# Kernel optimization log

Hardware: AMD Instinct MI355X
Metric: run time of the kernel (lower is better)

The kernel has to match this reference:

```python
import jax, jax.numpy as jnp
import numpy as np

C = 128; L = 2; LMAX = 3; NB = 8
R_MAX = 5.0; P_CUT = 5.0; AVG_NEI = 16.0
DELTA_K = 0.2; K_CUT = 0.6; NKRBF = 128; DP = 8
B_GRAPHS = 8; N_ATOMS = 3200; N_EDGES = 51200; NEL = 10
SKIP = (2.0 + 1.0) ** -0.5  # skip_connection_factor with use_ewald=True
_LOFLM_NP = np.repeat(np.arange(4), [1, 3, 5, 7])  # l index of each of 16 lm slots
LOFLM = jnp.asarray(_LOFLM_NP)
LM1H = jnp.asarray(np.eye(4, dtype=np.float32)[_LOFLM_NP])  # [16,4] one-hot lm->l


def _k_grid_np():
    r = np.arange(-3, 4)
    g = np.stack(np.meshgrid(r, r, r, indexing='ij'), -1).reshape(-1, 3).astype(np.float32) * DELTA_K
    return g[np.linalg.norm(g, axis=1) <= K_CUT + 1e-6]  # [K,3], K=123


def _k_rbf_np(kg):
    d = np.linalg.norm(kg, axis=1)
    c = np.linspace(0.0, K_CUT, NKRBF).astype(np.float32)
    w = c[1] - c[0]
    return np.exp(-0.5 * ((d[:, None] - c[None, :]) / w) ** 2).astype(np.float32)


def _sph_harm(u):
    # real spherical harmonics, e3nn 'component' normalization, l=0..3 -> 16 comps
    x, y, z = u[:, 0], u[:, 1], u[:, 2]
    s3, s5, s15 = 3.0 ** 0.5, 5.0 ** 0.5, 15.0 ** 0.5
    c70, c105, c42, c7 = 70.0 ** 0.5 / 4.0, 105.0 ** 0.5, 42.0 ** 0.5 / 4.0, 7.0 ** 0.5 / 2.0
    comps = [jnp.ones_like(x),
             s3 * x, s3 * y, s3 * z,
             s15 * x * y, s15 * y * z, 0.5 * s5 * (3 * z * z - 1.0), s15 * x * z, 0.5 * s15 * (x * x - y * y),
             c70 * y * (3 * x * x - y * y), c105 * x * y * z, c42 * y * (5 * z * z - 1.0),
             c7 * z * (5 * z * z - 3.0), c42 * x * (5 * z * z - 1.0), 0.5 * c105 * z * (x * x - y * y),
             c70 * x * (x * x - 3 * y * y)]
    return jnp.stack(comps, axis=-1)


def _radial(r):
    # Bessel basis * polynomial cutoff envelope (p=5)
    n = jnp.arange(1, NB + 1, dtype=r.dtype)
    rb = jnp.sqrt(2.0 / R_MAX) * jnp.sin(n * jnp.pi * r[:, None] / R_MAX) / jnp.maximum(r, 1e-9)[:, None]
    uu = jnp.clip(r / R_MAX, 0.0, 1.0)
    p = P_CUT
    env = 1.0 - (p + 1.0) * (p + 2.0) / 2.0 * uu ** 5 + p * (p + 2.0) * uu ** 6 - p * (p + 1.0) / 2.0 * uu ** 7
    env = env * (r < R_MAX)
    return rb * env[:, None]


def _forward(positions, node_attrs, shifts, edge_index, batch, kgrid, krbf, W_embed, atomic_E, rW1, rb1, rW2, rb2, rW3, rb3, rW4, Wup, w2, w3, Wmix, Wr0, Wr1a, Wr1b, Wdown, WupE, Wpre1, bpre1, Wpre2, bpre2, Wm1, bm1, Wm2, bm2):
    silu = jax.nn.silu
    src, dst = edge_index[0], edge_index[1]
    vec = positions[dst] - positions[src] + shifts            # [E,3]
    r = jnp.linalg.norm(vec, axis=1)
    uvec = vec / jnp.maximum(r, 1e-9)[:, None]
    Y = _sph_harm(uvec)                                       # [E,16]
    ef = _radial(r)                                           # [E,8]
    h = node_attrs @ W_embed                                  # [N,C]
    e0 = jax.ops.segment_sum(node_attrs @ atomic_E, batch, num_segments=B_GRAPHS)
    # Ewald precompute (shared across layers, as in the torch code: dot/sinc computed once)
    dot = positions @ kgrid.T                                 # [N,K]
    sd = jnp.prod(jnp.sinc(0.5 * DELTA_K * positions), axis=1, keepdims=True)  # [N,1]
    cosd = sd * jnp.cos(dot)
    sind = sd * jnp.sin(dot)
    kdown = krbf @ Wdown                                      # [K,DP]
    energy = e0
    for i in range(L):
        # ---- Ewald block ----
        hres = h + silu(h @ Wpre1[i] + bpre1[i]) @ Wpre2[i] + bpre2[i]
        kfilter = kdown @ WupE[i]                             # [K,C]
        sfr = jax.ops.segment_sum(hres[:, None, :] * cosd[:, :, None], batch, num_segments=B_GRAPHS)  # [B,K,C]
        sfi = jax.ops.segment_sum(hres[:, None, :] * sind[:, :, None], batch, num_segments=B_GRAPHS)
        he = 0.01 * (jnp.einsum('nk,nkc->nc', cosd, (sfr * kfilter)[batch])
                     + jnp.einsum('nk,nkc->nc', sind, (sfi * kfilter)[batch]))
        he = silu(he @ Wm1[i] + bm1[i])
        he = silu(he @ Wm2[i] + bm2[i])
        # ---- equivariant interaction (channelwise TP with SH, radial-MLP weights) ----
        hu = h @ Wup[i]
        w = silu(ef @ rW1[i] + rb1[i])
        w = silu(w @ rW2[i] + rb2[i])
        w = silu(w @ rW3[i] + rb3[i])
        w = (w @ rW4[i]).reshape(-1, C, LMAX + 1)             # [E,C,4] per-(channel,l) weights
        we = jnp.take(w, LOFLM, axis=2)                       # [E,C,16]
        msg = we * hu[src][:, :, None] * Y[:, None, :]        # [E,C,16]
        A = jax.ops.segment_sum(msg, dst, num_segments=positions.shape[0]) / AVG_NEI  # [N,C,16]
        # ---- product basis (invariant contractions up to correlation 3) + residual sc ----
        scal = A[:, :, 0]
        inv2 = jnp.einsum('ncs,sl->ncl', A * A, LM1H)         # [N,C,4] per-l norms
        feats = scal + jnp.einsum('ncl,lc->nc', inv2, w2[i]) + scal * jnp.einsum('ncl,lc->nc', inv2, w3[i])
        hprod = feats @ Wmix[i] + h
        h = SKIP * (hprod + he)
        # ---- readout ----
        if i < L - 1:
            node_e = (h @ Wr0)[:, 0]
        else:
            node_e = (silu(h @ Wr1a) @ Wr1b)[:, 0]
        energy = energy + jax.ops.segment_sum(node_e, batch, num_segments=B_GRAPHS)
    return energy  # [B]


def setup_inputs() -> dict:
    ks = jax.random.split(jax.random.key(0), 32)
    def rn(i, shape, scale):
        return jax.random.normal(ks[i], shape, jnp.float32) * scale
    d = {}
    d['positions'] = jax.random.normal(ks[0], (N_ATOMS, 3), jnp.float32)
    d['node_attrs'] = jax.random.uniform(ks[1], (N_ATOMS, NEL), dtype=jnp.float32)
    d['shifts'] = jnp.zeros((N_EDGES, 3), jnp.float32)
    d['edge_index'] = jax.random.randint(ks[2], (2, N_EDGES), 0, N_ATOMS)
    d['batch'] = jnp.sort(jax.random.randint(ks[3], (N_ATOMS,), 0, B_GRAPHS))
    kg = _k_grid_np()
    d['kgrid'] = jnp.asarray(kg)
    d['krbf'] = jnp.asarray(_k_rbf_np(kg))
    d['W_embed'] = rn(4, (NEL, C), NEL ** -0.5)
    d['atomic_E'] = rn(5, (NEL,), 1.0)
    d['rW1'] = rn(6, (L, NB, 64), NB ** -0.5)
    d['rb1'] = jnp.zeros((L, 64), jnp.float32)
    d['rW2'] = rn(7, (L, 64, 64), 64 ** -0.5)
    d['rb2'] = jnp.zeros((L, 64), jnp.float32)
    d['rW3'] = rn(8, (L, 64, 64), 64 ** -0.5)
    d['rb3'] = jnp.zeros((L, 64), jnp.float32)
    d['rW4'] = rn(9, (L, 64, C * (LMAX + 1)), 64 ** -0.5)
    d['Wup'] = rn(10, (L, C, C), C ** -0.5)
    d['w2'] = rn(11, (L, LMAX + 1, C), 0.1)
    d['w3'] = rn(12, (L, LMAX + 1, C), 0.1)
    d['Wmix'] = rn(13, (L, C, C), C ** -0.5)
    d['Wr0'] = rn(14, (C, 1), C ** -0.5)
    d['Wr1a'] = rn(15, (C, 16), C ** -0.5)
    d['Wr1b'] = rn(16, (16, 1), 16 ** -0.5)
    d['Wdown'] = rn(17, (NKRBF, DP), NKRBF ** -0.5)
    d['WupE'] = rn(18, (L, DP, C), DP ** -0.5)
    d['Wpre1'] = rn(19, (L, C, C), C ** -0.5)
    d['bpre1'] = jnp.zeros((L, C), jnp.float32)
    d['Wpre2'] = rn(20, (L, C, C), C ** -0.5)
    d['bpre2'] = jnp.zeros((L, C), jnp.float32)
    d['Wm1'] = rn(21, (L, C, C), C ** -0.5)
    d['bm1'] = jnp.zeros((L, C), jnp.float32)
    d['Wm2'] = rn(22, (L, C, C), C ** -0.5)
    d['bm2'] = jnp.zeros((L, C), jnp.float32)
    return d


def reference(positions, node_attrs, shifts, edge_index, batch, kgrid, krbf, W_embed, atomic_E, rW1, rb1, rW2, rb2, rW3, rb3, rW4, Wup, w2, w3, Wmix, Wr0, Wr1a, Wr1b, Wdown, WupE, Wpre1, bpre1, Wpre2, bpre2, Wm1, bm1, Wm2, bm2):
    return _forward(positions, node_attrs, shifts, edge_index, batch, kgrid, krbf, W_embed, atomic_E, rW1, rb1, rW2, rb2, rW3, rb3, rW4, Wup, w2, w3, Wmix, Wr0, Wr1a, Wr1b, Wdown, WupE, Wpre1, bpre1, Wpre2, bpre2, Wm1, bm1, Wm2, bm2)
```

## Files before the change

### kernel.cpp

```cpp
#include <hip/hip_runtime.h>
#include <hip/hip_bf16.h>
#include <math.h>

constexpr int NA  = 3200;
constexpr int NE  = 51200;
constexpr int C   = 128;
constexpr int NK  = 123;
constexpr int NKP = 128;
constexpr int BG  = 8;
constexpr int SFSPLIT = 8;
constexpr float SKIPF = 0.57735026918962576f;
constexpr float AVGN  = 16.0f;
constexpr size_t SFSZ = (size_t)BG * NK * C;

__device__ __forceinline__ float dsilu(float x) { return x / (1.0f + expf(-x)); }

__device__ __forceinline__ unsigned short f2bf(float f) {
    unsigned int u = __float_as_uint(f);
    unsigned int r = (u + 0x7fffu + ((u >> 16) & 1u)) >> 16;
    return (unsigned short)r;
}
__device__ __forceinline__ float bf2f(unsigned short s) {
    return __uint_as_float(((unsigned int)s) << 16);
}

typedef __attribute__((ext_vector_type(8))) short short8;
typedef __attribute__((ext_vector_type(4))) float f32x4;

template <int K, int ACT, int OBF16, int LB = 0>
__global__ __launch_bounds__(256, 4) void gemm_kernel(
    const float* __restrict__ X, const float* __restrict__ W,
    const float* __restrict__ bias, void* __restrict__ outv,
    int M, int N)
{
    if (LB) {
        int L = blockIdx.z;
        W += (size_t)L * K * N;
        if (bias) bias += (size_t)L * N;
        outv = OBF16 ? (void*)((unsigned short*)outv + (size_t)L * M * N)
                     : (void*)((float*)outv + (size_t)L * M * N);
    }
    constexpr int K4 = K / 4;
    constexpr int BK  = (K < 64) ? K : 64;
    constexpr int BK4 = BK / 4;
    constexpr int BK4P = BK4 + 1;
    __shared__ float As[64 * BK4P * 4];
    __shared__ float Bs[BK * 64];
    const int tid = threadIdx.x;
    const int m0 = blockIdx.x * 64;
    const int n0 = blockIdx.y * 64;

    const float4* X4 = (const float4*)X;
    const float4* W4 = (const float4*)W;
    float4* As4 = (float4*)As;
    float4* Bs4 = (float4*)Bs;
    const int N4 = N >> 2;

    const int tx = tid & 15;
    const int ty = tid >> 4;
    float acc[4][4];
#pragma unroll
    for (int i = 0; i < 4; i++)
#pragma unroll
        for (int j = 0; j < 4; j++) acc[i][j] = 0.0f;

    for (int k0 = 0; k0 < K4; k0 += BK4) {
        if (k0) __syncthreads();
        for (int idx = tid; idx < 64 * BK4; idx += 256) {
            int r = idx / BK4, k4 = idx - r * BK4;
            As4[r * BK4P + k4] = X4[(size_t)(m0 + r) * K4 + k0 + k4];
        }
        for (int idx = tid; idx < BK * 16; idx += 256) {
            int kr = idx >> 4, c4 = idx & 15;
            Bs4[idx] = W4[(size_t)(k0 * 4 + kr) * N4 + (n0 >> 2) + c4];
        }
        __syncthreads();

#pragma unroll 4
        for (int k4 = 0; k4 < BK4; k4++) {
            float a[4][4];
#pragma unroll
            for (int i = 0; i < 4; i++) {
                float4 av = As4[(ty * 4 + i) * BK4P + k4];
                a[i][0] = av.x; a[i][1] = av.y; a[i][2] = av.z; a[i][3] = av.w;
            }
#pragma unroll
            for (int kk = 0; kk < 4; kk++) {
                float4 bv = Bs4[(k4 * 4 + kk) * 16 + tx];
#pragma unroll
                for (int i = 0; i < 4; i++) {
                    acc[i][0] += a[i][kk] * bv.x;
                    acc[i][1] += a[i][kk] * bv.y;
                    acc[i][2] += a[i][kk] * bv.z;
                    acc[i][3] += a[i][kk] * bv.w;
                }
            }
        }
    }

    float4 bv = make_float4(0.f, 0.f, 0.f, 0.f);
    if (bias) bv = ((const float4*)bias)[(n0 >> 2) + tx];
#pragma unroll
    for (int i = 0; i < 4; i++) {
        int row = m0 + ty * 4 + i;
        size_t o = (size_t)row * N + n0 + tx * 4;
        float4 v;
        v.x = acc[i][0] + bv.x; v.y = acc[i][1] + bv.y;
        v.z = acc[i][2] + bv.z; v.w = acc[i][3] + bv.w;
        if (ACT) { v.x = dsilu(v.x); v.y = dsilu(v.y); v.z = dsilu(v.z); v.w = dsilu(v.w); }
        if (OBF16) {
            ushort4 pk;
            pk.x = f2bf(v.x); pk.y = f2bf(v.y); pk.z = f2bf(v.z); pk.w = f2bf(v.w);
            *(ushort4*)((unsigned short*)outv + o) = pk;
        } else {
            *(float4*)((float*)outv + o) = v;
        }
    }
}

__global__ __launch_bounds__(256, 2) void k_pre(
    const float* __restrict__ h,
    const unsigned short* __restrict__ W1t, const float* __restrict__ b1,
    const unsigned short* __restrict__ Wut,
    const unsigned short* __restrict__ W2t, const float* __restrict__ b2,
    float* __restrict__ hu, float* __restrict__ hres)
{
    constexpr int MT = 32, ASH = 136;
    __shared__ unsigned short Xs[MT * ASH];
    __shared__ unsigned short Ts[MT * ASH];
    __shared__ unsigned short Ws[128 * ASH];
    const int tid = threadIdx.x;
    const int m0 = blockIdx.x * MT;

    for (int idx = tid; idx < MT * 32; idx += 256) {
        int r = idx >> 5, c4 = idx & 31;
        float4 v = ((const float4*)h)[(size_t)(m0 + r) * 32 + c4];
        ushort4 pk;
        pk.x = f2bf(v.x); pk.y = f2bf(v.y); pk.z = f2bf(v.z); pk.w = f2bf(v.w);
        *(ushort4*)(Xs + r * ASH + c4 * 4) = pk;
    }
    for (int idx = tid; idx < 128 * 16; idx += 256) {
        int r = idx >> 4, s = idx & 15;
        *(short8*)(Ws + r * ASH + s * 8) = ((const short8*)W1t)[(size_t)r * 16 + s];
    }
    __syncthreads();

    const int wave = tid >> 6;
    const int lane = tid & 63;
    const int q = lane >> 4;
    const int l16 = lane & 15;
    const int mh = (wave & 1) * 16;
    const int nh = (wave >> 1) * 64;

    f32x4 acc[4];
#pragma unroll
    for (int ni = 0; ni < 4; ni++) acc[ni] = (f32x4){0.f, 0.f, 0.f, 0.f};
#pragma unroll
    for (int kc = 0; kc < 4; kc++) {
        short8 a = *(const short8*)(Xs + (mh + l16) * ASH + kc * 32 + q * 8);
#pragma unroll
        for (int ni = 0; ni < 4; ni++) {
            short8 b = *(const short8*)(Ws + (nh + ni * 16 + l16) * ASH + kc * 32 + q * 8);
            acc[ni] = __builtin_amdgcn_mfma_f32_16x16x32_bf16(a, b, acc[ni], 0, 0, 0);
        }
    }
#pragma unroll
    for (int ni = 0; ni < 4; ni++) {
        float bv = b1[nh + ni * 16 + l16];
#pragma unroll
        for (int r = 0; r < 4; r++)
            Ts[(mh + q * 4 + r) * ASH + nh + ni * 16 + l16] = f2bf(dsilu(acc[ni][r] + bv));
    }
    __syncthreads();
    for (int idx = tid; idx < 128 * 16; idx += 256) {
        int r = idx >> 4, s = idx & 15;
        *(short8*)(Ws + r * ASH + s * 8) = ((const short8*)Wut)[(size_t)r * 16 + s];
    }
    __syncthreads();
#pragma unroll
    for (int ni = 0; ni < 4; ni++) acc[ni] = (f32x4){0.f, 0.f, 0.f, 0.f};
#pragma unroll
    for (int kc = 0; kc < 4; kc++) {
        short8 a = *(const short8*)(Xs + (mh + l16) * ASH + kc * 32 + q * 8);
#pragma unroll
        for (int ni = 0; ni < 4; ni++) {
            short8 b = *(const short8*)(Ws + (nh + ni * 16 + l16) * ASH + kc * 32 + q * 8);
            acc[ni] = __builtin_amdgcn_mfma_f32_16x16x32_bf16(a, b, acc[ni], 0, 0, 0);
        }
    }
#pragma unroll
    for (int ni = 0; ni < 4; ni++) {
#pragma unroll
        for (int r = 0; r < 4; r++)
            hu[(size_t)(m0 + mh + q * 4 + r) * C + nh + ni * 16 + l16] = acc[ni][r];
    }
    __syncthreads();
    for (int idx = tid; idx < 128 * 16; idx += 256) {
        int r = idx >> 4, s = idx & 15;
        *(short8*)(Ws + r * ASH + s * 8) = ((const short8*)W2t)[(size_t)r * 16 + s];
    }
    __syncthreads();
#pragma unroll
    for (int ni = 0; ni < 4; ni++) acc[ni] = (f32x4){0.f, 0.f, 0.f, 0.f};
#pragma unroll
    for (int kc = 0; kc < 4; kc++) {
        short8 a = *(const short8*)(Ts + (mh + l16) * ASH + kc * 32 + q * 8);
#pragma unroll
        for (int ni = 0; ni < 4; ni++) {
            short8 b = *(const short8*)(Ws + (nh + ni * 16 + l16) * ASH + kc * 32 + q * 8);
            acc[ni] = __builtin_amdgcn_mfma_f32_16x16x32_bf16(a, b, acc[ni], 0, 0, 0);
        }
    }
#pragma unroll
    for (int ni = 0; ni < 4; ni++) {
        float bv = b2[nh + ni * 16 + l16];
#pragma unroll
        for (int r = 0; r < 4; r++) {
            int row = m0 + mh + q * 4 + r;
            int col = nh + ni * 16 + l16;
            hres[(size_t)row * C + col] = acc[ni][r] + bv + h[(size_t)row * C + col];
        }
    }
}

__global__ __launch_bounds__(128, 2) void k_mlp_mfma(
    const unsigned short* __restrict__ X, const unsigned short* __restrict__ Wbase,
    const float* __restrict__ bbase, unsigned short* __restrict__ out)
{
    constexpr int MT = 128, AS = 72;
    __shared__ unsigned short Als[MT * AS];
    __shared__ unsigned short Bls[64 * AS];
    const int tid = threadIdx.x;
    const int m0 = blockIdx.x * MT;
    const int layer = (m0 >= NE) ? 1 : 0;
    const unsigned short* Wt = Wbase + (size_t)layer * 64 * 64;
    const float* bias = bbase + (size_t)layer * 64;

    for (int idx = tid; idx < MT * 8; idx += 128) {
        int r = idx >> 3, s = idx & 7;
        *(short8*)(Als + r * AS + s * 8) = ((const short8*)X)[(size_t)(m0 + r) * 8 + s];
    }
    for (int idx = tid; idx < 64 * 8; idx += 128) {
        int r = idx >> 3, s = idx & 7;
        *(short8*)(Bls + r * AS + s * 8) = ((const short8*)Wt)[(size_t)r * 8 + s];
    }
    __syncthreads();

    const int wave = tid >> 6;
    const int lane = tid & 63;
    const int q = lane >> 4;
    const int l16 = lane & 15;
    const int mw = wave * 64;

    f32x4 acc[4][4];
#pragma unroll
    for (int mi = 0; mi < 4; mi++)
#pragma unroll
        for (int ni = 0; ni < 4; ni++) acc[mi][ni] = (f32x4){0.f, 0.f, 0.f, 0.f};

#pragma unroll
    for (int kc = 0; kc < 2; kc++) {
        short8 a[4], b[4];
#pragma unroll
        for (int mi = 0; mi < 4; mi++)
            a[mi] = *(const short8*)(Als + (mw + mi * 16 + l16) * AS + kc * 32 + q * 8);
#pragma unroll
        for (int ni = 0; ni < 4; ni++)
            b[ni] = *(const short8*)(Bls + (ni * 16 + l16) * AS + kc * 32 + q * 8);
#pragma unroll
        for (int mi = 0; mi < 4; mi++)
#pragma unroll
            for (int ni = 0; ni < 4; ni++)
                acc[mi][ni] = __builtin_amdgcn_mfma_f32_16x16x32_bf16(a[mi], b[ni], acc[mi][ni], 0, 0, 0);
    }

#pragma unroll
    for (int ni = 0; ni < 4; ni++) {
        float bv = bias[ni * 16 + l16];
#pragma unroll
        for (int mi = 0; mi < 4; mi++) {
#pragma unroll
            for (int r = 0; r < 4; r++) {
                int e = m0 + mw + mi * 16 + q * 4 + r;
                int n = ni * 16 + l16;
                out[(size_t)e * 64 + n] = f2bf(dsilu(acc[mi][ni][r] + bv));
            }
        }
    }
}

__global__ __launch_bounds__(256, 2) void k_wbuf_mfma(
    const unsigned short* __restrict__ X, const unsigned short* __restrict__ W4base,
    unsigned short* __restrict__ wbuf)
{
    constexpr int MT = 256, NT = 64, AS = 72;
    __shared__ unsigned short Als[MT * AS];
    __shared__ unsigned short Bls[NT * AS];
    const int tid = threadIdx.x;
    const int m0 = blockIdx.x * MT;
    const int n0 = blockIdx.y * NT;
    const int layer = (m0 >= NE) ? 1 : 0;
    const unsigned short* W4t = W4base + (size_t)layer * 512 * 64;

    for (int idx = tid; idx < MT * 8; idx += 256) {
        int r = idx >> 3, s = idx & 7;
        *(short8*)(Als + r * AS + s * 8) = ((const short8*)X)[(size_t)(m0 + r) * 8 + s];
    }
    for (int idx = tid; idx < NT * 8; idx += 256) {
        int r = idx >> 3, s = idx & 7;
        *(short8*)(Bls + r * AS + s * 8) = ((const short8*)W4t)[(size_t)(n0 + r) * 8 + s];
    }
    __syncthreads();

    const int wave = tid >> 6;
    const int lane = tid & 63;
    const int q = lane >> 4;
    const int l16 = lane & 15;
    const int mw = wave * 64;

    f32x4 acc[4][4];
#pragma unroll
    for (int mi = 0; mi < 4; mi++)
#pragma unroll
        for (int ni = 0; ni < 4; ni++) acc[mi][ni] = (f32x4){0.f, 0.f, 0.f, 0.f};

#pragma unroll
    for (int kc = 0; kc < 2; kc++) {
        short8 a[4], b[4];
#pragma unroll
        for (int mi = 0; mi < 4; mi++)
            a[mi] = *(const short8*)(Als + (mw + mi * 16 + l16) * AS + kc * 32 + q * 8);
#pragma unroll
        for (int ni = 0; ni < 4; ni++)
            b[ni] = *(const short8*)(Bls + (ni * 16 + l16) * AS + kc * 32 + q * 8);
#pragma unroll
        for (int mi = 0; mi < 4; mi++)
#pragma unroll
            for (int ni = 0; ni < 4; ni++)
                acc[mi][ni] = __builtin_amdgcn_mfma_f32_16x16x32_bf16(a[mi], b[ni], acc[mi][ni], 0, 0, 0);
    }

#pragma unroll
    for (int mi = 0; mi < 4; mi++) {
#pragma unroll
        for (int ni = 0; ni < 4; ni++) {
#pragma unroll
            for (int r = 0; r < 4; r++) {
                int e = m0 + mw + mi * 16 + q * 4 + r;
                int n = n0 + ni * 16 + l16;
                wbuf[(size_t)e * 512 + n] = f2bf(acc[mi][ni][r]);
            }
        }
    }
}

constexpr int TK0 = NA;
constexpr int TK1 = TK0 + 8;
constexpr int TK2 = TK1 + 512;
constexpr int TK3 = TK2 + 64;
constexpr int TK4 = TK3 + 64;
constexpr int TK5 = TK4 + 256;
constexpr int TK6 = TK5 + 256;
constexpr int TK7 = TK6 + 256;
constexpr int TK8 = TK7 + 256;
constexpr int TK9 = TK8 + 256;
constexpr int TKEND = TK9 + 1;

__device__ __forceinline__ float sincn(float x) {
    float px = 3.14159265358979323846f * x;
    return (fabsf(px) < 1e-8f) ? 1.0f : (sinf(px) / px);
}

__device__ __forceinline__ void convT128_task(
    const float* __restrict__ W, unsigned short* __restrict__ Wt, int idx)
{
    int layer = idx >> 14, rem = idx & 16383;
    int n = rem >> 7, k = rem & 127;
    Wt[((size_t)layer << 14) + (n << 7) + k] = f2bf(W[((size_t)layer << 14) + (k << 7) + n]);
}

__global__ __launch_bounds__(128) void k_setup(
    const float* __restrict__ na, const float* __restrict__ Wemb,
    const float* __restrict__ aE, const int* __restrict__ batch,
    const float* __restrict__ pos, const float* __restrict__ kgrid,
    const float* __restrict__ krbf, const float* __restrict__ Wdown,
    const float* __restrict__ rW4, const float* __restrict__ rW2,
    const float* __restrict__ rW3, const float* __restrict__ Wm1,
    const float* __restrict__ Wm2, const float* __restrict__ Wpre1,
    const float* __restrict__ Wpre2, const float* __restrict__ Wup,
    float* __restrict__ h, float* __restrict__ e0buf,
    float* __restrict__ cosd, float* __restrict__ sind,
    unsigned short* __restrict__ cosdb, unsigned short* __restrict__ sindb,
    float* __restrict__ kdwn,
    unsigned short* __restrict__ W4bt, unsigned short* __restrict__ W2bt,
    unsigned short* __restrict__ W3bt, unsigned short* __restrict__ Wm1bt,
    unsigned short* __restrict__ Wm2bt, unsigned short* __restrict__ Wpre1bt,
    unsigned short* __restrict__ Wpre2bt, unsigned short* __restrict__ Wupbt,
    int* __restrict__ gs)
{
    const int bx = blockIdx.x;
    const int t = threadIdx.x;
    __shared__ int cnt[BG];

    if (bx < TK0) {
        int n = bx, c = t;
        float s = 0.f;
#pragma unroll
        for (int k = 0; k < 10; k++) s += na[n * 10 + k] * Wemb[k * C + c];
        h[(size_t)n * C + c] = s;
        if (c == 0) {
            float e = 0.f;
#pragma unroll
            for (int k = 0; k < 10; k++) e += na[n * 10 + k] * aE[k];
            e0buf[n] = e;
        }
        float p0 = pos[n * 3 + 0], p1 = pos[n * 3 + 1], p2 = pos[n * 3 + 2];
        float sd = sincn(0.1f * p0) * sincn(0.1f * p1) * sincn(0.1f * p2);
        int k = t;
        float cv = 0.f, sv = 0.f;
        if (k < NK) {
            float d = p0 * kgrid[k * 3 + 0] + p1 * kgrid[k * 3 + 1] + p2 * kgrid[k * 3 + 2];
            float sn, cs;
            sincosf(d, &sn, &cs);
            cv = sd * cs;
            sv = sd * sn;
        }
        cosd[(size_t)n * NKP + k] = cv;
        sind[(size_t)n * NKP + k] = sv;
        cosdb[(size_t)n * NKP + k] = f2bf(cv);
        sindb[(size_t)n * NKP + k] = f2bf(sv);
    } else if (bx < TK1) {
        int slot = (bx - TK0) * 128 + t;
        if (slot < NK * 8) {
            int k = slot >> 3, j = slot & 7;
            float s = 0.f;
            for (int r = 0; r < 128; r++) s += krbf[k * 128 + r] * Wdown[r * 8 + j];
            kdwn[slot] = s;
        }
    } else if (bx < TK2) {
        int idx = (bx - TK1) * 128 + t;
        int layer = idx >> 15, rem = idx & 32767;
        int n = rem >> 6, k = rem & 63;
        W4bt[((size_t)layer * 512 + n) * 64 + k] = f2bf(rW4[((size_t)layer * 64 + k) * 512 + n]);
    } else if (bx < TK3) {
        int idx = (bx - TK2) * 128 + t;
        int layer = idx >> 12, rem = idx & 4095;
        int n = rem >> 6, k = rem & 63;
        W2bt[((size_t)layer * 64 + n) * 64 + k] = f2bf(rW2[((size_t)layer * 64 + k) * 64 + n]);
    } else if (bx < TK4) {
        int idx = (bx - TK3) * 128 + t;
        int layer = idx >> 12, rem = idx & 4095;
        int n = rem >> 6, k = rem & 63;
        W3bt[((size_t)layer * 64 + n) * 64 + k] = f2bf(rW3[((size_t)layer * 64 + k) * 64 + n]);
    } else if (bx < TK5) {
        convT128_task(Wm1, Wm1bt, (bx - TK4) * 128 + t);
    } else if (bx < TK6) {
        convT128_task(Wm2, Wm2bt, (bx - TK5) * 128 + t);
    } else if (bx < TK7) {
        convT128_task(Wpre1, Wpre1bt, (bx - TK6) * 128 + t);
    } else if (bx < TK8) {
        convT128_task(Wpre2, Wpre2bt, (bx - TK7) * 128 + t);
    } else if (bx < TK9) {
        convT128_task(Wup, Wupbt, (bx - TK8) * 128 + t);
    } else {
        if (t < BG) cnt[t] = 0;
        __syncthreads();
        for (int n = t; n < NA; n += 128) atomicAdd(&cnt[batch[n]], 1);
        __syncthreads();
        if (t == 0) {
            int s = 0;
            for (int b = 0; b < BG; b++) { gs[b] = s; s += cnt[b]; }
            gs[BG] = s;
        }
    }
}

__global__ __launch_bounds__(256) void k_count(const int* __restrict__ eidx, int* __restrict__ deg)
{
    int e = blockIdx.x * 256 + threadIdx.x;
    if (e < NE) atomicAdd(&deg[eidx[NE + e]], 1);
}

__global__ __launch_bounds__(1024) void k_scan(
    const int* __restrict__ deg, int* __restrict__ offs, int* __restrict__ cursor)
{
    __shared__ int sc[1024];
    int tid = threadIdx.x;
    int base = tid * 4;
    int v[4]; int s = 0;
#pragma unroll
    for (int i = 0; i < 4; i++) {
        int idx = base + i;
        int d = (idx < NA) ? deg[idx] : 0;
        v[i] = s; s += d;
    }
    sc[tid] = s;
    __syncthreads();
    for (int ofs = 1; ofs < 1024; ofs <<= 1) {
        int t = (tid >= ofs) ? sc[tid - ofs] : 0;
        __syncthreads();
        sc[tid] += t;
        __syncthreads();
    }
    int excl = (tid > 0) ? sc[tid - 1] : 0;
#pragma unroll
    for (int i = 0; i < 4; i++) {
        int idx = base + i;
        if (idx < NA) { int o = excl + v[i]; offs[idx] = o; cursor[idx] = o; }
    }
    if (tid == 1023) offs[NA] = sc[1023];
}

__global__ __launch_bounds__(256) void k_fill(
    const int* __restrict__ eidx, int* __restrict__ cursor,
    int* __restrict__ perm, int* __restrict__ srcP)
{
    int e = blockIdx.x * 256 + threadIdx.x;
    if (e < NE) {
        int d = eidx[NE + e];
        int p = atomicAdd(&cursor[d], 1);
        perm[p] = e;
        srcP[p] = eidx[e];
    }
}

__global__ __launch_bounds__(256) void k_edge_geom(
    const float* __restrict__ pos, const float* __restrict__ shifts,
    const int* __restrict__ eidx, const int* __restrict__ perm,
    float* __restrict__ Y, float* __restrict__ ef)
{
    int j = blockIdx.x * 256 + threadIdx.x;
    if (j >= NE) return;
    int e = perm[j];
    int s = eidx[e], d = eidx[NE + e];
    float vx = pos[d * 3 + 0] - pos[s * 3 + 0] + shifts[e * 3 + 0];
    float vy = pos[d * 3 + 1] - pos[s * 3 + 1] + shifts[e * 3 + 1];
    float vz = pos[d * 3 + 2] - pos[s * 3 + 2] + shifts[e * 3 + 2];
    float r = sqrtf(vx * vx + vy * vy + vz * vz);
// ... 401 lines not shown
    for (int n = n0 + t; n < n1; n += 256)
        s += e0buf[n] + nebuf[n] + nebuf[NA + n];
#pragma unroll
    for (int o = 32; o; o >>= 1) s += __shfl_down(s, o, 64);
    __shared__ float red[4];
    if ((t & 63) == 0) red[t >> 6] = s;
    __syncthreads();
    if (t == 0) Eout[b] = red[0] + red[1] + red[2] + red[3];
}

constexpr size_t NAC   = (size_t)NA * C;
constexpr size_t F_COSD = 0;
constexpr size_t F_SIND = F_COSD + (size_t)NA * NKP;
constexpr size_t F_Y    = F_SIND + (size_t)NA * NKP;
constexpr size_t F_EF   = F_Y + (size_t)NE * 16;
constexpr size_t F_H    = F_EF + (size_t)NE * 8;
constexpr size_t F_HN   = F_H + NAC;
constexpr size_t F_HRES = F_HN + NAC;
constexpr size_t F_T1   = F_HRES + NAC;
constexpr size_t F_HE2  = F_T1 + NAC;
constexpr size_t F_HU   = F_HE2 + NAC;
constexpr size_t F_TA   = F_HU + NAC;
constexpr size_t F_TB   = F_TA + (size_t)NE * 64;
constexpr size_t F_WTS  = F_TB + (size_t)NE * 64;
constexpr size_t F_W    = F_WTS + 128 * 1024;
constexpr size_t F_SFR  = F_W + (size_t)NE * 512;
constexpr size_t F_SFI  = F_SFR + SFSZ;
constexpr size_t F_SFP  = F_SFI + SFSZ;
constexpr size_t F_KD   = F_SFP + 2 * (size_t)SFSPLIT * SFSZ;
constexpr size_t F_E0   = F_KD + 1024;
constexpr size_t F_NE   = F_E0 + NA;
constexpr size_t F_CB   = F_NE + 2 * (size_t)NA;
constexpr size_t F_SB   = F_CB + (size_t)NA * 64;
constexpr size_t F_END  = F_SB + (size_t)NA * 64;
constexpr size_t I_BASE = ((F_END * 4 + 255) / 256) * 256;

extern "C" void kernel_launch(void* const* d_in, const int* in_sizes, int n_in,
                              void* d_out, int out_size, void* d_ws, size_t ws_size,
                              hipStream_t stream) {
    const float* pos    = (const float*)d_in[0];
    const float* na     = (const float*)d_in[1];
    const float* shifts = (const float*)d_in[2];
    const int*   eidx   = (const int*)d_in[3];
    const int*   batch  = (const int*)d_in[4];
    const float* kgrid  = (const float*)d_in[5];
    const float* krbf   = (const float*)d_in[6];
    const float* Wemb   = (const float*)d_in[7];
    const float* aE     = (const float*)d_in[8];
    const float* rW1    = (const float*)d_in[9];
    const float* rb1    = (const float*)d_in[10];
    const float* rW2    = (const float*)d_in[11];
    const float* rb2    = (const float*)d_in[12];
    const float* rW3    = (const float*)d_in[13];
    const float* rb3    = (const float*)d_in[14];
    const float* rW4    = (const float*)d_in[15];
    const float* Wup    = (const float*)d_in[16];
    const float* w2     = (const float*)d_in[17];
    const float* w3     = (const float*)d_in[18];
    const float* Wmix   = (const float*)d_in[19];
    const float* Wr0    = (const float*)d_in[20];
    const float* Wr1a   = (const float*)d_in[21];
    const float* Wr1b   = (const float*)d_in[22];
    const float* Wdown  = (const float*)d_in[23];
    const float* WupE   = (const float*)d_in[24];
    const float* Wpre1  = (const float*)d_in[25];
    const float* bpre1  = (const float*)d_in[26];
    const float* Wpre2  = (const float*)d_in[27];
    const float* bpre2  = (const float*)d_in[28];
    const float* Wm1    = (const float*)d_in[29];
    const float* bm1    = (const float*)d_in[30];
    const float* Wm2    = (const float*)d_in[31];
    const float* bm2    = (const float*)d_in[32];

    float* fw = (float*)d_ws;
    float* cosd = fw + F_COSD;
    float* sind = fw + F_SIND;
    float* Ybuf = fw + F_Y;
    float* efb  = fw + F_EF;
    float* h    = fw + F_H;
    float* hn   = fw + F_HN;
    float* hres = fw + F_HRES;
    float* he2  = fw + F_HE2;
    float* hu   = fw + F_HU;
    unsigned short* tA   = (unsigned short*)(fw + F_TA);
    unsigned short* hbuf = (unsigned short*)(fw + F_TB);
    unsigned short* W4bt = (unsigned short*)(fw + F_WTS);
    unsigned short* W2bt  = W4bt + (size_t)2 * 512 * 64;
    unsigned short* W3bt  = W2bt + (size_t)2 * 64 * 64;
    unsigned short* Wm1bt = W3bt + (size_t)2 * 64 * 64;
    unsigned short* Wm2bt = Wm1bt + (size_t)2 * 128 * 128;
    unsigned short* Wp1bt = Wm2bt + (size_t)2 * 128 * 128;
    unsigned short* Wp2bt = Wp1bt + (size_t)2 * 128 * 128;
    unsigned short* Wupbt = Wp2bt + (size_t)2 * 128 * 128;
    unsigned short* wbuf = (unsigned short*)(fw + F_W);
    unsigned short* sfrT = (unsigned short*)(fw + F_SFR);
    unsigned short* sfiT = (unsigned short*)(fw + F_SFI);
    float* sfp  = fw + F_SFP;
    float* kdwn = fw + F_KD;
    float* e0buf = fw + F_E0;
    float* nebuf = fw + F_NE;
    unsigned short* cosdb = (unsigned short*)(fw + F_CB);
    unsigned short* sindb = (unsigned short*)(fw + F_SB);

    int* ip     = (int*)((char*)d_ws + I_BASE);
    int* deg    = ip;
    int* offs   = ip + NA;
    int* cursor = ip + 2 * NA + 1;
    int* perm   = ip + 3 * NA + 1;
    int* srcP   = perm + NE;
    int* gs     = srcP + NE;

    float* Eout = (float*)d_out;

    hipMemsetAsync(deg, 0, NA * sizeof(int), stream);

    k_setup<<<TKEND, 128, 0, stream>>>(
        na, Wemb, aE, batch, pos, kgrid, krbf, Wdown,
        rW4, rW2, rW3, Wm1, Wm2, Wpre1, Wpre2, Wup,
        h, e0buf, cosd, sind, cosdb, sindb, kdwn,
        W4bt, W2bt, W3bt, Wm1bt, Wm2bt, Wp1bt, Wp2bt, Wupbt, gs);
    k_count<<<NE / 256, 256, 0, stream>>>(eidx, deg);
    k_scan<<<1, 1024, 0, stream>>>(deg, offs, cursor);
    k_fill<<<NE / 256, 256, 0, stream>>>(eidx, cursor, perm, srcP);
    k_edge_geom<<<NE / 256, 256, 0, stream>>>(pos, shifts, eidx, perm, Ybuf, efb);

    gemm_kernel<8, 1, 1, 1><<<dim3(NE / 64, 1, 2), 256, 0, stream>>>(
        efb, rW1, rb1, hbuf, NE, 64);
    k_mlp_mfma<<<2 * NE / 128, 128, 0, stream>>>(hbuf, W2bt, rb2, tA);
    k_mlp_mfma<<<2 * NE / 128, 128, 0, stream>>>(tA, W3bt, rb3, hbuf);
    k_wbuf_mfma<<<dim3(2 * NE / 256, 512 / 64), 256, 0, stream>>>(hbuf, W4bt, wbuf);

    const dim3 gSF(BG, 4, SFSPLIT);
    const dim3 gRT(8, BG);
    const dim3 gHE(16, BG);

    for (int i = 0; i < 2; i++) {
        const float* bpre1_i = bpre1 + (size_t)i * C;
        const float* bpre2_i = bpre2 + (size_t)i * C;
        const float* WupE_i  = WupE + (size_t)i * 8 * C;
        const float* bm1_i   = bm1 + (size_t)i * C;
        const float* bm2_i   = bm2 + (size_t)i * C;
        const float* w2_i    = w2 + (size_t)i * 4 * C;
        const float* w3_i    = w3 + (size_t)i * 4 * C;
        const float* Wmix_i  = Wmix + (size_t)i * C * C;
        const unsigned short* Wm1bt_i = Wm1bt + (size_t)i * 128 * 128;
        const unsigned short* Wm2bt_i = Wm2bt + (size_t)i * 128 * 128;
        const unsigned short* Wp1bt_i = Wp1bt + (size_t)i * 128 * 128;
        const unsigned short* Wp2bt_i = Wp2bt + (size_t)i * 128 * 128;
        const unsigned short* Wupbt_i = Wupbt + (size_t)i * 128 * 128;
        const unsigned short* wbuf_i = wbuf + (size_t)i * NE * 512;

        k_pre<<<NA / 32, 256, 0, stream>>>(h, Wp1bt_i, bpre1_i, Wupbt_i,
                                           Wp2bt_i, bpre2_i, hu, hres);

        k_sf<<<gSF, 256, 0, stream>>>(hres, cosd, sind, gs, kdwn, WupE_i, sfp);
        k_sfredT<<<gRT, 256, 0, stream>>>(sfp, sfrT, sfiT);
        k_he_mlp<<<gHE, 256, 0, stream>>>(cosdb, sindb, sfrT, sfiT, gs,
                                          Wm1bt_i, bm1_i, Wm2bt_i, bm2_i, he2);

        k_gather_mix<<<NA, 128, 0, stream>>>(wbuf_i, hu, Ybuf, srcP, offs,
                                             w2_i, w3_i, Wmix_i, h, he2,
                                             Wr0, Wr1a, Wr1b, (i == 0) ? 0 : 1,
                                             hn, nebuf + (size_t)i * NA);

        float* tmp = h; h = hn; hn = tmp;
    }

    k_reduceE<<<BG, 256, 0, stream>>>(e0buf, nebuf, gs, Eout);
}
```

Baseline: 338.9 us.

## Fuse the four-stage radial edge MLP into one MFMA kernel

Replaces the fp32 first-layer GEMM, two per-layer MFMA MLP kernels and the final wbuf projection kernel with a single kernel. Each block keeps a 128-edge tile's intermediate activations in shared memory through all four layers, and the first layer now runs on bf16 MFMA using a zero-padded transposed weight built in setup. This removes three launches and the global round-trips of the hidden activations. In exchange, the first layer loses fp32 precision, the larger shared-memory footprint limits occupancy, and the output projection loops over eight column tiles within one block instead of spreading them across the grid.

```diff
diff --git a/kernel.cpp b/kernel.cpp
--- a/kernel.cpp
+++ b/kernel.cpp
@@ -27,97 +27,6 @@
 typedef __attribute__((ext_vector_type(8))) short short8;
 typedef __attribute__((ext_vector_type(4))) float f32x4;
 
-template <int K, int ACT, int OBF16, int LB = 0>
-__global__ __launch_bounds__(256, 4) void gemm_kernel(
-    const float* __restrict__ X, const float* __restrict__ W,
-    const float* __restrict__ bias, void* __restrict__ outv,
-    int M, int N)
-{
-    if (LB) {
-        int L = blockIdx.z;
-        W += (size_t)L * K * N;
-        if (bias) bias += (size_t)L * N;
-        outv = OBF16 ? (void*)((unsigned short*)outv + (size_t)L * M * N)
-                     : (void*)((float*)outv + (size_t)L * M * N);
-    }
-    constexpr int K4 = K / 4;
-    constexpr int BK  = (K < 64) ? K : 64;
-    constexpr int BK4 = BK / 4;
-    constexpr int BK4P = BK4 + 1;
-    __shared__ float As[64 * BK4P * 4];
-    __shared__ float Bs[BK * 64];
-    const int tid = threadIdx.x;
-    const int m0 = blockIdx.x * 64;
-    const int n0 = blockIdx.y * 64;
-
-    const float4* X4 = (const float4*)X;
-    const float4* W4 = (const float4*)W;
-    float4* As4 = (float4*)As;
-    float4* Bs4 = (float4*)Bs;
-    const int N4 = N >> 2;
-
-    const int tx = tid & 15;
-    const int ty = tid >> 4;
-    float acc[4][4];
-#pragma unroll
-    for (int i = 0; i < 4; i++)
-#pragma unroll
-        for (int j = 0; j < 4; j++) acc[i][j] = 0.0f;
-
-    for (int k0 = 0; k0 < K4; k0 += BK4) {
-        if (k0) __syncthreads();
-        for (int idx = tid; idx < 64 * BK4; idx += 256) {
-            int r = idx / BK4, k4 = idx - r * BK4;
-            As4[r * BK4P + k4] = X4[(size_t)(m0 + r) * K4 + k0 + k4];
-        }
-        for (int idx = tid; idx < BK * 16; idx += 256) {
-            int kr = idx >> 4, c4 = idx & 15;
-            Bs4[idx] = W4[(size_t)(k0 * 4 + kr) * N4 + (n0 >> 2) + c4];
-        }
-        __syncthreads();
-
-#pragma unroll 4
-        for (int k4 = 0; k4 < BK4; k4++) {
-            float a[4][4];
-#pragma unroll
-            for (int i = 0; i < 4; i++) {
-                float4 av = As4[(ty * 4 + i) * BK4P + k4];
-                a[i][0] = av.x; a[i][1] = av.y; a[i][2] = av.z; a[i][3] = av.w;
-            }
-#pragma unroll
-            for (int kk = 0; kk < 4; kk++) {
-                float4 bv = Bs4[(k4 * 4 + kk) * 16 + tx];
-#pragma unroll
-                for (int i = 0; i < 4; i++) {
-                    acc[i][0] += a[i][kk] * bv.x;
-                    acc[i][1] += a[i][kk] * bv.y;
-                    acc[i][2] += a[i][kk] * bv.z;
-                    acc[i][3] += a[i][kk] * bv.w;
-                }
-            }
-        }
-    }
-
-    float4 bv = make_float4(0.f, 0.f, 0.f, 0.f);
-    if (bias) bv = ((const float4*)bias)[(n0 >> 2) + tx];
-#pragma unroll
-    for (int i = 0; i < 4; i++) {
-        int row = m0 + ty * 4 + i;
-        size_t o = (size_t)row * N + n0 + tx * 4;
-        float4 v;
-        v.x = acc[i][0] + bv.x; v.y = acc[i][1] + bv.y;
-        v.z = acc[i][2] + bv.z; v.w = acc[i][3] + bv.w;
-        if (ACT) { v.x = dsilu(v.x); v.y = dsilu(v.y); v.z = dsilu(v.z); v.w = dsilu(v.w); }
-        if (OBF16) {
-            ushort4 pk;
-            pk.x = f2bf(v.x); pk.y = f2bf(v.y); pk.z = f2bf(v.z); pk.w = f2bf(v.w);
-            *(ushort4*)((unsigned short*)outv + o) = pk;
-        } else {
-            *(float4*)((float*)outv + o) = v;
-        }
-    }
-}
-
 __global__ __launch_bounds__(256, 2) void k_pre(
     const float* __restrict__ h,
     const unsigned short* __restrict__ W1t, const float* __restrict__ b1,
@@ -223,26 +132,44 @@
     }
 }
 
-__global__ __launch_bounds__(128, 2) void k_mlp_mfma(
-    const unsigned short* __restrict__ X, const unsigned short* __restrict__ Wbase,
-    const float* __restrict__ bbase, unsigned short* __restrict__ out)
-{
-    constexpr int MT = 128, AS = 72;
-    __shared__ unsigned short Als[MT * AS];
-    __shared__ unsigned short Bls[64 * AS];
+__global__ __launch_bounds__(256, 2) void k_edge_mlp(
+    const float* __restrict__ efb,
+    const unsigned short* __restrict__ W1bt, const float* __restrict__ rb1,
+    const unsigned short* __restrict__ W2bt, const float* __restrict__ rb2,
+    const unsigned short* __restrict__ W3bt, const float* __restrict__ rb3,
+    const unsigned short* __restrict__ W4bt,
+    unsigned short* __restrict__ wbuf)
+{
+    constexpr int TS = 72;
+    constexpr int AS0 = 40;
+    __shared__ __align__(16) char smem[56320];
+    unsigned short* A0 = (unsigned short*)smem;
+    unsigned short* T1 = (unsigned short*)(smem + 10240);
+    unsigned short* T2 = (unsigned short*)(smem + 28672);
+    unsigned short* WB = (unsigned short*)(smem + 47104);
     const int tid = threadIdx.x;
-    const int m0 = blockIdx.x * MT;
-    const int layer = (m0 >= NE) ? 1 : 0;
-    const unsigned short* Wt = Wbase + (size_t)layer * 64 * 64;
-    const float* bias = bbase + (size_t)layer * 64;
-
-    for (int idx = tid; idx < MT * 8; idx += 128) {
-        int r = idx >> 3, s = idx & 7;
-        *(short8*)(Als + r * AS + s * 8) = ((const short8*)X)[(size_t)(m0 + r) * 8 + s];
-    }
-    for (int idx = tid; idx < 64 * 8; idx += 128) {
-        int r = idx >> 3, s = idx & 7;
-        *(short8*)(Bls + r * AS + s * 8) = ((const short8*)Wt)[(size_t)r * 8 + s];
+    const int nb = NE / 128;
+    const int layer = (blockIdx.x >= nb) ? 1 : 0;
+    const size_t m0 = (size_t)(blockIdx.x - layer * nb) * 128;
+
+    {
+        int idx = tid;
+        int r = idx >> 1, hf = idx & 1;
+        float4 v = ((const float4*)efb)[(m0 + r) * 2 + hf];
+        ushort4 pk;
+        pk.x = f2bf(v.x); pk.y = f2bf(v.y); pk.z = f2bf(v.z); pk.w = f2bf(v.w);
+        *(ushort4*)(A0 + r * AS0 + hf * 4) = pk;
+    }
+    const short8 z8 = (short8){0,0,0,0,0,0,0,0};
+    for (int idx = tid; idx < 384; idx += 256) {
+        int r = idx / 3, s = idx - r * 3;
+        *(short8*)(A0 + r * AS0 + 8 + s * 8) = z8;
+    }
+    {
+        int idx = tid;
+        int r = idx >> 2, s = idx & 3;
+        *(short8*)(WB + r * TS + s * 8) =
+            ((const short8*)(W1bt + (size_t)layer * 64 * 32))[r * 4 + s];
     }
     __syncthreads();
 
@@ -250,107 +177,136 @@
     const int lane = tid & 63;
     const int q = lane >> 4;
     const int l16 = lane & 15;
-    const int mw = wave * 64;
-
-    f32x4 acc[4][4];
-#pragma unroll
-    for (int mi = 0; mi < 4; mi++)
+    const int mw = wave * 32;
+
+    const float* b1 = rb1 + layer * 64;
+    const float* b2 = rb2 + layer * 64;
+    const float* b3 = rb3 + layer * 64;
+
+    f32x4 acc[2][4];
+#pragma unroll
+    for (int mi = 0; mi < 2; mi++)
 #pragma unroll
         for (int ni = 0; ni < 4; ni++) acc[mi][ni] = (f32x4){0.f, 0.f, 0.f, 0.f};
-
+#pragma unroll
+    for (int mi = 0; mi < 2; mi++) {
+        short8 a = *(const short8*)(A0 + (mw + mi * 16 + l16) * AS0 + q * 8);
+#pragma unroll
+        for (int ni = 0; ni < 4; ni++) {
+            short8 b = *(const short8*)(WB + (ni * 16 + l16) * TS + q * 8);
+            acc[mi][ni] = __builtin_amdgcn_mfma_f32_16x16x32_bf16(a, b, acc[mi][ni], 0, 0, 0);
+        }
+    }
+#pragma unroll
+    for (int ni = 0; ni < 4; ni++) {
+        float bv = b1[ni * 16 + l16];
+#pragma unroll
+        for (int mi = 0; mi < 2; mi++)
+#pragma unroll
+            for (int r = 0; r < 4; r++)
+                T1[(mw + mi * 16 + q * 4 + r) * TS + ni * 16 + l16] = f2bf(dsilu(acc[mi][ni][r] + bv));
+    }
+    __syncthreads();
+    for (int idx = tid; idx < 512; idx += 256) {
+        int r = idx >> 3, s = idx & 7;
+        *(short8*)(WB + r * TS + s * 8) =
+            ((const short8*)(W2bt + (size_t)layer * 64 * 64))[r * 8 + s];
+    }
+    __syncthreads();
+#pragma unroll
+    for (int mi = 0; mi < 2; mi++)
+#pragma unroll
+        for (int ni = 0; ni < 4; ni++) acc[mi][ni] = (f32x4){0.f, 0.f, 0.f, 0.f};
 #pragma unroll
     for (int kc = 0; kc < 2; kc++) {
-        short8 a[4], b[4];
-#pragma unroll
-        for (int mi = 0; mi < 4; mi++)
-            a[mi] = *(const short8*)(Als + (mw + mi * 16 + l16) * AS + kc * 32 + q * 8);
-#pragma unroll
-        for (int ni = 0; ni < 4; ni++)
-            b[ni] = *(const short8*)(Bls + (ni * 16 + l16) * AS + kc * 32 + q * 8);
-#pragma unroll
-        for (int mi = 0; mi < 4; mi++)
+#pragma unroll
+        for (int mi = 0; mi < 2; mi++) {
+            short8 a = *(const short8*)(T1 + (mw + mi * 16 + l16) * TS + kc * 32 + q * 8);
+#pragma unroll
+            for (int ni = 0; ni < 4; ni++) {
+                short8 b = *(const short8*)(WB + (ni * 16 + l16) * TS + kc * 32 + q * 8);
+                acc[mi][ni] = __builtin_amdgcn_mfma_f32_16x16x32_bf16(a, b, acc[mi][ni], 0, 0, 0);
+            }
+        }
+    }
+#pragma unroll
+    for (int ni = 0; ni < 4; ni++) {
+        float bv = b2[ni * 16 + l16];
+#pragma unroll
+        for (int mi = 0; mi < 2; mi++)
+#pragma unroll
+            for (int r = 0; r < 4; r++)
+                T2[(mw + mi * 16 + q * 4 + r) * TS + ni * 16 + l16] = f2bf(dsilu(acc[mi][ni][r] + bv));
+    }
+    __syncthreads();
+    for (int idx = tid; idx < 512; idx += 256) {
+        int r = idx >> 3, s = idx & 7;
+        *(short8*)(WB + r * TS + s * 8) =
+            ((const short8*)(W3bt + (size_t)layer * 64 * 64))[r * 8 + s];
+    }
+    __syncthreads();
+#pragma unroll
+    for (int mi = 0; mi < 2; mi++)
+#pragma unroll
+        for (int ni = 0; ni < 4; ni++) acc[mi][ni] = (f32x4){0.f, 0.f, 0.f, 0.f};
+#pragma unroll
+    for (int kc = 0; kc < 2; kc++) {
+#pragma unroll
+        for (int mi = 0; mi < 2; mi++) {
+            short8 a = *(const short8*)(T2 + (mw + mi * 16 + l16) * TS + kc * 32 + q * 8);
+#pragma unroll
+            for (int ni = 0; ni < 4; ni++) {
+                short8 b = *(const short8*)(WB + (ni * 16 + l16) * TS + kc * 32 + q * 8);
+                acc[mi][ni] = __builtin_amdgcn_mfma_f32_16x16x32_bf16(a, b, acc[mi][ni], 0, 0, 0);
+            }
+        }
+    }
+#pragma unroll
+    for (int ni = 0; ni < 4; ni++) {
+        float bv = b3[ni * 16 + l16];
+#pragma unroll
+        for (int mi = 0; mi < 2; mi++)
+#pragma unroll
+            for (int r = 0; r < 4; r++)
+                T1[(mw + mi * 16 + q * 4 + r) * TS + ni * 16 + l16] = f2bf(dsilu(acc[mi][ni][r] + bv));
+    }
+
+    const unsigned short* W4l = W4bt + (size_t)layer * 512 * 64;
+    unsigned short* wout = wbuf + ((size_t)layer * NE + m0) * 512;
+#pragma unroll 1
+    for (int nt = 0; nt < 8; nt++) {
+        __syncthreads();
+        for (int idx = tid; idx < 512; idx += 256) {
+            int r = idx >> 3, s = idx & 7;
+            *(short8*)(WB + r * TS + s * 8) = ((const short8*)W4l)[(nt * 64 + r) * 8 + s];
+        }
+        __syncthreads();
+#pragma unroll
+        for (int mi = 0; mi < 2; mi++)
+#pragma unroll
+            for (int ni = 0; ni < 4; ni++) acc[mi][ni] = (f32x4){0.f, 0.f, 0.f, 0.f};
+#pragma unroll
+        for (int kc = 0; kc < 2; kc++) {
+#pragma unroll
+            for (int mi = 0; mi < 2; mi++) {
+                short8 a = *(const short8*)(T1 + (mw + mi * 16 + l16) * TS + kc * 32 + q * 8);
+#pragma unroll
+                for (int ni = 0; ni < 4; ni++) {
+                    short8 b = *(const short8*)(WB + (ni * 16 + l16) * TS + kc * 32 + q * 8);
+                    acc[mi][ni] = __builtin_amdgcn_mfma_f32_16x16x32_bf16(a, b, acc[mi][ni], 0, 0, 0);
+                }
+            }
+        }
+#pragma unroll
+        for (int mi = 0; mi < 2; mi++)
 #pragma unroll
             for (int ni = 0; ni < 4; ni++)
-                acc[mi][ni] = __builtin_amdgcn_mfma_f32_16x16x32_bf16(a[mi], b[ni], acc[mi][ni], 0, 0, 0);
-    }
-
-#pragma unroll
-    for (int ni = 0; ni < 4; ni++) {
-        float bv = bias[ni * 16 + l16];
-#pragma unroll
-        for (int mi = 0; mi < 4; mi++) {
-#pragma unroll
-            for (int r = 0; r < 4; r++) {
-                int e = m0 + mw + mi * 16 + q * 4 + r;
-                int n = ni * 16 + l16;
-                out[(size_t)e * 64 + n] = f2bf(dsilu(acc[mi][ni][r] + bv));
-            }
-        }
-    }
-}
-
-__global__ __launch_bounds__(256, 2) void k_wbuf_mfma(
-    const unsigned short* __restrict__ X, const unsigned short* __restrict__ W4base,
-    unsigned short* __restrict__ wbuf)
-{
-    constexpr int MT = 256, NT = 64, AS = 72;
-    __shared__ unsigned short Als[MT * AS];
-    __shared__ unsigned short Bls[NT * AS];
-    const int tid = threadIdx.x;
-    const int m0 = blockIdx.x * MT;
-    const int n0 = blockIdx.y * NT;
-    const int layer = (m0 >= NE) ? 1 : 0;
-    const unsigned short* W4t = W4base + (size_t)layer * 512 * 64;
-
-    for (int idx = tid; idx < MT * 8; idx += 256) {
-        int r = idx >> 3, s = idx & 7;
-        *(short8*)(Als + r * AS + s * 8) = ((const short8*)X)[(size_t)(m0 + r) * 8 + s];
-    }
-    for (int idx = tid; idx < NT * 8; idx += 256) {
-        int r = idx >> 3, s = idx & 7;
-        *(short8*)(Bls + r * AS + s * 8) = ((const short8*)W4t)[(size_t)(n0 + r) * 8 + s];
-    }
-    __syncthreads();
-
-    const int wave = tid >> 6;
-    const int lane = tid & 63;
-    const int q = lane >> 4;
-    const int l16 = lane & 15;
-    const int mw = wave * 64;
-
-    f32x4 acc[4][4];
-#pragma unroll
-    for (int mi = 0; mi < 4; mi++)
-#pragma unroll
-        for (int ni = 0; ni < 4; ni++) acc[mi][ni] = (f32x4){0.f, 0.f, 0.f, 0.f};
-
-#pragma unroll
-    for (int kc = 0; kc < 2; kc++) {
-        short8 a[4], b[4];
-#pragma unroll
-        for (int mi = 0; mi < 4; mi++)
-            a[mi] = *(const short8*)(Als + (mw + mi * 16 + l16) * AS + kc * 32 + q * 8);
-#pragma unroll
-        for (int ni = 0; ni < 4; ni++)
-            b[ni] = *(const short8*)(Bls + (ni * 16 + l16) * AS + kc * 32 + q * 8);
-#pragma unroll
-        for (int mi = 0; mi < 4; mi++)
-#pragma unroll
-            for (int ni = 0; ni < 4; ni++)
-                acc[mi][ni] = __builtin_amdgcn_mfma_f32_16x16x32_bf16(a[mi], b[ni], acc[mi][ni], 0, 0, 0);
-    }
-
-#pragma unroll
-    for (int mi = 0; mi < 4; mi++) {
-#pragma unroll
-        for (int ni = 0; ni < 4; ni++) {
-#pragma unroll
-            for (int r = 0; r < 4; r++) {
-                int e = m0 + mw + mi * 16 + q * 4 + r;
-                int n = n0 + ni * 16 + l16;
-                wbuf[(size_t)e * 512 + n] = f2bf(acc[mi][ni][r]);
-            }
-        }
+#pragma unroll
+                for (int r = 0; r < 4; r++) {
+                    int row = mw + mi * 16 + q * 4 + r;
+                    int col = nt * 64 + ni * 16 + l16;
+                    wout[(size_t)row * 512 + col] = f2bf(acc[mi][ni][r]);
+                }
     }
 }
 
@@ -359,7 +315,8 @@
 constexpr int TK2 = TK1 + 512;
 constexpr int TK3 = TK2 + 64;
 constexpr int TK4 = TK3 + 64;
-constexpr int TK5 = TK4 + 256;
+constexpr int TK4b = TK4 + 32;
+constexpr int TK5 = TK4b + 256;
 constexpr int TK6 = TK5 + 256;
 constexpr int TK7 = TK6 + 256;
 constexpr int TK8 = TK7 + 256;
@@ -385,17 +342,19 @@
     const float* __restrict__ pos, const float* __restrict__ kgrid,
     const float* __restrict__ krbf, const float* __restrict__ Wdown,
     const float* __restrict__ rW4, const float* __restrict__ rW2,
-    const float* __restrict__ rW3, const float* __restrict__ Wm1,
-    const float* __restrict__ Wm2, const float* __restrict__ Wpre1,
-    const float* __restrict__ Wpre2, const float* __restrict__ Wup,
+    const float* __restrict__ rW3, const float* __restrict__ rW1,
+    const float* __restrict__ Wm1, const float* __restrict__ Wm2,
+    const float* __restrict__ Wpre1, const float* __restrict__ Wpre2,
+    const float* __restrict__ Wup,
     float* __restrict__ h, float* __restrict__ e0buf,
     float* __restrict__ cosd, float* __restrict__ sind,
     unsigned short* __restrict__ cosdb, unsigned short* __restrict__ sindb,
     float* __restrict__ kdwn,
     unsigned short* __restrict__ W4bt, unsigned short* __restrict__ W2bt,
-    unsigned short* __restrict__ W3bt, unsigned short* __restrict__ Wm1bt,
-    unsigned short* __restrict__ Wm2bt, unsigned short* __restrict__ Wpre1bt,
-    unsigned short* __restrict__ Wpre2bt, unsigned short* __restrict__ Wupbt,
+    unsigned short* __restrict__ W3bt, unsigned short* __restrict__ W1bt,
+    unsigned short* __restrict__ Wm1bt, unsigned short* __restrict__ Wm2bt,
+    unsigned short* __restrict__ Wpre1bt, unsigned short* __restrict__ Wpre2bt,
+    unsigned short* __restrict__ Wupbt,
     int* __restrict__ gs)
 {
     const int bx = blockIdx.x;
@@ -452,8 +411,14 @@
         int layer = idx >> 12, rem = idx & 4095;
         int n = rem >> 6, k = rem & 63;
         W3bt[((size_t)layer * 64 + n) * 64 + k] = f2bf(rW3[((size_t)layer * 64 + k) * 64 + n]);
+    } else if (bx < TK4b) {
+        int idx = (bx - TK4) * 128 + t;
+        int layer = idx >> 11, rem = idx & 2047;
+        int n = rem >> 5, k = rem & 31;
+        W1bt[((size_t)layer * 64 + n) * 32 + k] =
+            (k < 8) ? f2bf(rW1[((size_t)layer * 8 + k) * 64 + n]) : (unsigned short)0;
     } else if (bx < TK5) {
-        convT128_task(Wm1, Wm1bt, (bx - TK4) * 128 + t);
+        convT128_task(Wm1, Wm1bt, (bx - TK4b) * 128 + t);
     } else if (bx < TK6) {
         convT128_task(Wm2, Wm2bt, (bx - TK5) * 128 + t);
     } else if (bx < TK7) {
@@ -1021,8 +986,6 @@
     float* hres = fw + F_HRES;
     float* he2  = fw + F_HE2;
     float* hu   = fw + F_HU;
-    unsigned short* tA   = (unsigned short*)(fw + F_TA);
-    unsigned short* hbuf = (unsigned short*)(fw + F_TB);
     unsigned short* W4bt = (unsigned short*)(fw + F_WTS);
     unsigned short* W2bt  = W4bt + (size_t)2 * 512 * 64;
     unsigned short* W3bt  = W2bt + (size_t)2 * 64 * 64;
@@ -1031,6 +994,7 @@
     unsigned short* Wp1bt = Wm2bt + (size_t)2 * 128 * 128;
     unsigned short* Wp2bt = Wp1bt + (size_t)2 * 128 * 128;
     unsigned short* Wupbt = Wp2bt + (size_t)2 * 128 * 128;
+    unsigned short* W1bt  = Wupbt + (size_t)2 * 128 * 128;
     unsigned short* wbuf = (unsigned short*)(fw + F_W);
     unsigned short* sfrT = (unsigned short*)(fw + F_SFR);
     unsigned short* sfiT = (unsigned short*)(fw + F_SFI);
@@ -1055,19 +1019,16 @@
 
     k_setup<<<TKEND, 128, 0, stream>>>(
         na, Wemb, aE, batch, pos, kgrid, krbf, Wdown,
-        rW4, rW2, rW3, Wm1, Wm2, Wpre1, Wpre2, Wup,
+        rW4, rW2, rW3, rW1, Wm1, Wm2, Wpre1, Wpre2, Wup,
         h, e0buf, cosd, sind, cosdb, sindb, kdwn,
-        W4bt, W2bt, W3bt, Wm1bt, Wm2bt, Wp1bt, Wp2bt, Wupbt, gs);
+        W4bt, W2bt, W3bt, W1bt, Wm1bt, Wm2bt, Wp1bt, Wp2bt, Wupbt, gs);
     k_count<<<NE / 256, 256, 0, stream>>>(eidx, deg);
     k_scan<<<1, 1024, 0, stream>>>(deg, offs, cursor);
     k_fill<<<NE / 256, 256, 0, stream>>>(eidx, cursor, perm, srcP);
     k_edge_geom<<<NE / 256, 256, 0, stream>>>(pos, shifts, eidx, perm, Ybuf, efb);
 
-    gemm_kernel<8, 1, 1, 1><<<dim3(NE / 64, 1, 2), 256, 0, stream>>>(
-        efb, rW1, rb1, hbuf, NE, 64);
-    k_mlp_mfma<<<2 * NE / 128, 128, 0, stream>>>(hbuf, W2bt, rb2, tA);
-    k_mlp_mfma<<<2 * NE / 128, 128, 0, stream>>>(tA, W3bt, rb3, hbuf);
-    k_wbuf_mfma<<<dim3(2 * NE / 256, 512 / 64), 256, 0, stream>>>(hbuf, W4bt, wbuf);
+    k_edge_mlp<<<2 * NE / 128, 256, 0, stream>>>(efb, W1bt, rb1, W2bt, rb2,
+                                                 W3bt, rb3, W4bt, wbuf);
 
     const dim3 gSF(BG, 4, SFSPLIT);
     const dim3 gRT(8, BG);
```

Result: faster. 322.4 us (-4.9%).
